# Optimization experiments

Measured on AMD Instinct MI355X. Metric: run time of the kernel, lower is better.

The kernel has to match this reference:

```python
import jax, jax.numpy as jnp
import numpy as np
import itertools

B, G, FEAT, IMG = 2048, 8, 512, 1024
SCALES = list(range(G, 1, -1))  # [8,7,6,5,4,3,2]
SUBSAMPLE = 12


def setup_inputs() -> dict:
    key = jax.random.key(0)
    keys = jax.random.split(key, 1 + 2 * len(SCALES))
    rng = np.random.default_rng(0)
    inp = {"input": jax.random.normal(keys[0], (B, G, FEAT), dtype=jnp.float32)}
    for i, scale in enumerate(SCALES):
        perms = np.array(list(itertools.permutations(range(G), scale)), dtype=np.int32)
        n_sub = min(SUBSAMPLE, len(perms))
        sel = rng.choice(len(perms), n_sub, replace=False)
        inp[f"perms{i}"] = jnp.asarray(perms[sel])  # [n_sub, scale] int32
        lim = 1.0 / np.sqrt(scale * FEAT)
        inp[f"W{i}"] = jax.random.uniform(keys[1 + 2 * i], (IMG, scale * FEAT), minval=-lim, maxval=lim, dtype=jnp.float32)
        inp[f"b{i}"] = jax.random.uniform(keys[2 + 2 * i], (IMG,), minval=-lim, maxval=lim, dtype=jnp.float32)
    return inp


def _forward(input, perms_list, W_list, b_list):
    outs = []
    for perms, W, b in zip(perms_list, W_list, b_list):
        # gather: [B, n_sub, scale, FEAT] -> [B, n_sub, scale*FEAT]
        g = input[:, perms, :]
        g = g.reshape(g.shape[0], g.shape[1], -1)
        # batched linear over all subsamples, then mean over subsamples
        y = jnp.einsum('bsf,df->bsd', g, W) + b  # [B, n_sub, IMG]
        outs.append(y.mean(axis=1))
    return jnp.concatenate(outs, axis=1)  # [B, len(SCALES)*IMG]


def reference(input, perms0, W0, b0, perms1, W1, b1, perms2, W2, b2,
              perms3, W3, b3, perms4, W4, b4, perms5, W5, b5, perms6, W6, b6):
    perms_list = [perms0, perms1, perms2, perms3, perms4, perms5, perms6]
    W_list = [W0, W1, W2, W3, W4, W5, W6]
    b_list = [b0, b1, b2, b3, b4, b5, b6]
    return _forward(input, perms_list, W_list, b_list)
```

## Files before the change

kernel.cpp:

```cpp
#include <hip/hip_runtime.h>

typedef unsigned short u16;
typedef __bf16 bf16x8 __attribute__((ext_vector_type(8)));
typedef float f32x4 __attribute__((ext_vector_type(4)));

__device__ __forceinline__ u16 f2bf(float f) {
  unsigned int u = __float_as_uint(f);
  return (u16)((u + 0x7fffu + ((u >> 16) & 1u)) >> 16);
}


__global__ __launch_bounds__(256) void k_prep(
    const float* __restrict__ x,
    const int* p0, const int* p1, const int* p2, const int* p3,
    const int* p4, const int* p5, const int* p6,
    const float* W0, const float* W1, const float* W2, const float* W3,
    const float* W4, const float* W5, const float* W6,
    u16* __restrict__ Xb16, u16* __restrict__ Wtil) {
  __shared__ float sC[64];
  const int bid = blockIdx.x;
  const int t = threadIdx.x;
  if (bid < 1792) {
    const int r0 = bid << 2;
    const int i = r0 >> 10;
    const int scale = 8 - i;
    const int K = scale << 9;
    const int d0 = r0 - (i << 10);
    if (t < 64) {
      const int g = t >> 3, j = t & 7;
      float v = 0.f;
      if (j < scale) {
        const int* p = (i == 0) ? p0 : (i == 1) ? p1 : (i == 2) ? p2 :
                       (i == 3) ? p3 : (i == 4) ? p4 : (i == 5) ? p5 : p6;
        int cnt = 0;
        for (int s = 0; s < 12; ++s) cnt += (p[s * scale + j] == g) ? 1 : 0;
        v = (float)cnt * (1.0f / 12.0f);
      }
      sC[t] = v;
    }
    __syncthreads();
    const float* Wi = (i == 0) ? W0 : (i == 1) ? W1 : (i == 2) ? W2 :
                      (i == 3) ? W3 : (i == 4) ? W4 : (i == 5) ? W5 : W6;
    const int u = t & 63;
    const int gq = t >> 6;
    u16* dst = Wtil + ((size_t)r0 << 12);
    for (int r = 0; r < 4; ++r) {
      const float* wrow = Wi + (size_t)(d0 + r) * K;
      float a0[8], a1[8];
#pragma unroll
      for (int e = 0; e < 8; ++e) { a0[e] = 0.f; a1[e] = 0.f; }
      for (int j = 0; j < scale; ++j) {
        const float* wp = wrow + j * 512 + (u << 3);
        const float4 wa = *reinterpret_cast<const float4*>(wp);
        const float4 wb = *reinterpret_cast<const float4*>(wp + 4);
        const float c0 = sC[(gq << 4) + j];
        const float c1 = sC[(gq << 4) + 8 + j];
        a0[0] += c0 * wa.x; a0[1] += c0 * wa.y; a0[2] += c0 * wa.z; a0[3] += c0 * wa.w;
        a0[4] += c0 * wb.x; a0[5] += c0 * wb.y; a0[6] += c0 * wb.z; a0[7] += c0 * wb.w;
        a1[0] += c1 * wa.x; a1[1] += c1 * wa.y; a1[2] += c1 * wa.z; a1[3] += c1 * wa.w;
        a1[4] += c1 * wb.x; a1[5] += c1 * wb.y; a1[6] += c1 * wb.z; a1[7] += c1 * wb.w;
      }
      uint4 o0, o1;
      o0.x = (unsigned)f2bf(a0[0]) | ((unsigned)f2bf(a0[1]) << 16);
      o0.y = (unsigned)f2bf(a0[2]) | ((unsigned)f2bf(a0[3]) << 16);
      o0.z = (unsigned)f2bf(a0[4]) | ((unsigned)f2bf(a0[5]) << 16);
      o0.w = (unsigned)f2bf(a0[6]) | ((unsigned)f2bf(a0[7]) << 16);
      o1.x = (unsigned)f2bf(a1[0]) | ((unsigned)f2bf(a1[1]) << 16);
      o1.y = (unsigned)f2bf(a1[2]) | ((unsigned)f2bf(a1[3]) << 16);
      o1.z = (unsigned)f2bf(a1[4]) | ((unsigned)f2bf(a1[5]) << 16);
      o1.w = (unsigned)f2bf(a1[6]) | ((unsigned)f2bf(a1[7]) << 16);
      u16* drow = dst + ((size_t)r << 12) + (gq << 10) + (u << 3);
      *reinterpret_cast<uint4*>(drow) = o0;
      *reinterpret_cast<uint4*>(drow + 512) = o1;
    }
  } else {
    const int tid0 = ((bid - 1792) << 8) | t;
    const float4* X4 = reinterpret_cast<const float4*>(x);
    uint4* O = reinterpret_cast<uint4*>(Xb16);
#pragma unroll 4
    for (int it = 0; it < 16; ++it) {
      const int e = tid0 + (it << 16);
      const float4 a = X4[(size_t)e * 2];
      const float4 c = X4[(size_t)e * 2 + 1];
      uint4 o;
      o.x = (unsigned)f2bf(a.x) | ((unsigned)f2bf(a.y) << 16);
      o.y = (unsigned)f2bf(a.z) | ((unsigned)f2bf(a.w) << 16);
      o.z = (unsigned)f2bf(c.x) | ((unsigned)f2bf(c.y) << 16);
      o.w = (unsigned)f2bf(c.z) | ((unsigned)f2bf(c.w) << 16);
      O[e] = o;
    }
  }
}

__device__ __forceinline__ void gl_lds16(const u16* g, u16* l) {
  __builtin_amdgcn_global_load_lds(
      (const __attribute__((address_space(1))) void*)g,
      (__attribute__((address_space(3))) void*)l, 16, 0, 0);
}

#define WAIT_VM2   0x0F72
#define WAIT_VM0   0x0F70
#define WAIT_LGKM0 0xC07F

#define MFMA_Q(MB, NB, AV, BV)                                               \
  _Pragma("unroll")                                                          \
  for (int q_ = 0; q_ < 4; ++q_) {                                           \
    _Pragma("unroll")                                                        \
    for (int n_ = 0; n_ < 2; ++n_) {                                         \
      acc[(MB) + q_][(NB) + n_] = __builtin_amdgcn_mfma_f32_16x16x32_bf16(   \
          AV[q_][0], BV[n_][0], acc[(MB) + q_][(NB) + n_], 0, 0, 0);         \
      acc[(MB) + q_][(NB) + n_] = __builtin_amdgcn_mfma_f32_16x16x32_bf16(   \
          AV[q_][1], BV[n_][1], acc[(MB) + q_][(NB) + n_], 0, 0, 0);         \
    }                                                                        \
  }

#define RD_A4(DB, QB)                                                        \
  _Pragma("unroll")                                                          \
  for (int q_ = 0; q_ < 4; ++q_) {                                           \
    aR[q_][0] = *reinterpret_cast<const bf16x8*>(lds + (DB) + offA[(QB) + q_]);         \
    aR[q_][1] = *reinterpret_cast<const bf16x8*>(lds + (DB) + (offA[(QB) + q_] ^ 32));  \
  }

#define RD_B2(DB, ARR, FB)                                                   \
  _Pragma("unroll")                                                          \
  for (int n_ = 0; n_ < 2; ++n_) {                                           \
    ARR[n_][0] = *reinterpret_cast<const bf16x8*>(lds + (DB) + offB[(FB) + n_]);        \
    ARR[n_][1] = *reinterpret_cast<const bf16x8*>(lds + (DB) + (offB[(FB) + n_] ^ 32)); \
  }

__global__ __launch_bounds__(512, 2) void k_gemm(
    const u16* __restrict__ A, const u16* __restrict__ Bm,
    const float* b0, const float* b1, const float* b2, const float* b3,
    const float* b4, const float* b5, const float* b6,
    float* __restrict__ out) {
  __shared__ u16 lds[65536];
  const int bid = blockIdx.x;
  const int blockM = (bid & 7) * 256;
  const int blockN = (bid >> 3) * 256;

  const int tid = threadIdx.x;
  const int lane = tid & 63;
  const int wid = tid >> 6;
  const int wr = wid >> 2;
  const int wc = wid & 3;
  const int quad = lane >> 4;
  const int l15 = lane & 15;

  const int srow = tid >> 3;
  const int sslot = tid & 7;
  const int gch = (sslot - srow) & 7;
  const u16* gA0 = A + (size_t)(blockM + srow) * 4096 + gch * 8;
  const u16* gB0 = Bm + (size_t)(blockN + srow) * 4096 + gch * 8;

  int offA[8], offB[4];
#pragma unroll
  for (int q = 0; q < 8; ++q) {
    const int r = q * 16 + l15;
    offA[q] = wr * 8192 + r * 64 + ((quad + r) & 7) * 8;
  }
#pragma unroll
  for (int f = 0; f < 4; ++f) {
    const int r = (wc & 1) * 64 + f * 16 + l15;
    offB[f] = 16384 + (wc >> 1) * 8192 + r * 64 + ((quad + r) & 7) * 8;
  }

  f32x4 acc[8][4];
#pragma unroll
  for (int m = 0; m < 8; ++m)
#pragma unroll
    for (int n = 0; n < 4; ++n) {
      f32x4 z = {0.f, 0.f, 0.f, 0.f};
      acc[m][n] = z;
    }

  auto stage = [&](int mat, int h, int t, int db) {
    const u16* g = (mat ? gB0 : gA0) + (size_t)h * (128 * 4096) + (size_t)t * 64;
    u16* l = lds + db + mat * 16384 + h * 8192 + (tid << 3);
    gl_lds16(g, l);
    gl_lds16(g + (size_t)(64 * 4096), l + 4096);
  };

  stage(0, 0, 0, 0); stage(0, 1, 0, 0); stage(1, 0, 0, 0); stage(1, 1, 0, 0);
  stage(0, 0, 1, 32768);
  __builtin_amdgcn_s_waitcnt(WAIT_VM2);
  __builtin_amdgcn_s_barrier();

  bf16x8 aR[4][2], bL[2][2], bH[2][2];

  for (int j = 0; j < 32; ++j) {
    const int t1 = 2 * j + 1;
    const int t2 = (j < 31) ? 2 * j + 2 : 63;
    const int t3 = (j < 31) ? 2 * j + 3 : 63;

    RD_A4(0, 0) RD_B2(0, bL, 0)
    stage(0, 1, t1, 32768);
    __builtin_amdgcn_s_barrier();
    __builtin_amdgcn_s_waitcnt(WAIT_LGKM0);
    __builtin_amdgcn_s_setprio(1);
    MFMA_Q(0, 0, aR, bL)
    __builtin_amdgcn_s_setprio(0);
    __builtin_amdgcn_s_barrier();

    RD_B2(0, bH, 2)
    stage(1, 0, t1, 32768);
    __builtin_amdgcn_s_barrier();
    __builtin_amdgcn_s_waitcnt(WAIT_LGKM0);
    __builtin_amdgcn_s_setprio(1);
    MFMA_Q(0, 2, aR, bH)
    __builtin_amdgcn_s_setprio(0);
    __builtin_amdgcn_s_barrier();

    RD_A4(0, 4)
    stage(1, 1, t1, 32768);
    __builtin_amdgcn_s_barrier();
    __builtin_amdgcn_s_waitcnt(WAIT_LGKM0);
    __builtin_amdgcn_s_setprio(1);
    MFMA_Q(4, 2, aR, bH)
    __builtin_amdgcn_s_setprio(0);
    __builtin_amdgcn_s_barrier();

    stage(0, 0, t2, 0);
    __builtin_amdgcn_s_barrier();
    __builtin_amdgcn_s_setprio(1);
    MFMA_Q(4, 0, aR, bL)
    __builtin_amdgcn_s_setprio(0);
    __builtin_amdgcn_s_waitcnt(WAIT_VM2);
    __builtin_amdgcn_s_barrier();

    RD_A4(32768, 0) RD_B2(32768, bL, 0)
    stage(0, 1, t2, 0);
    __builtin_amdgcn_s_barrier();
    __builtin_amdgcn_s_waitcnt(WAIT_LGKM0);
    __builtin_amdgcn_s_setprio(1);
    MFMA_Q(0, 0, aR, bL)
    __builtin_amdgcn_s_setprio(0);
    __builtin_amdgcn_s_barrier();

    RD_B2(32768, bH, 2)
    stage(1, 0, t2, 0);
    __builtin_amdgcn_s_barrier();
    __builtin_amdgcn_s_waitcnt(WAIT_LGKM0);
    __builtin_amdgcn_s_setprio(1);
    MFMA_Q(0, 2, aR, bH)
    __builtin_amdgcn_s_setprio(0);
    __builtin_amdgcn_s_barrier();

    RD_A4(32768, 4)
    stage(1, 1, t2, 0);
    __builtin_amdgcn_s_barrier();
    __builtin_amdgcn_s_waitcnt(WAIT_LGKM0);
    __builtin_amdgcn_s_setprio(1);
    MFMA_Q(4, 2, aR, bH)
    __builtin_amdgcn_s_setprio(0);
    __builtin_amdgcn_s_barrier();

    stage(0, 0, t3, 32768);
    __builtin_amdgcn_s_barrier();
    __builtin_amdgcn_s_setprio(1);
    MFMA_Q(4, 0, aR, bL)
    __builtin_amdgcn_s_setprio(0);
    __builtin_amdgcn_s_waitcnt(WAIT_VM2);
    __builtin_amdgcn_s_barrier();
  }
  __builtin_amdgcn_s_waitcnt(WAIT_VM0);

  const int isc = blockN >> 10;
  const float* bi = (isc == 0) ? b0 : (isc == 1) ? b1 : (isc == 2) ? b2 :
                    (isc == 3) ? b3 : (isc == 4) ? b4 : (isc == 5) ? b5 : b6;
#pragma unroll
  for (int nf = 0; nf < 4; ++nf) {
    const int ncol = blockN + wc * 64 + nf * 16 + l15;
    const float bias = bi[ncol & 1023];
#pragma unroll
    for (int mq = 0; mq < 8; ++mq) {
      const int mbase = blockM + wr * 128 + mq * 16 + quad * 4;
#pragma unroll
      for (int reg = 0; reg < 4; ++reg)
        out[(size_t)(mbase + reg) * 7168 + ncol] = acc[mq][nf][reg] + bias;
    }
  }
}

extern "C" void kernel_launch(void* const* d_in, const int* in_sizes, int n_in,
                              void* d_out, int out_size, void* d_ws, size_t ws_size,
                              hipStream_t stream) {
  const float* input = (const float*)d_in[0];
  const int* perms[7];
  const float* W[7];
  const float* bias[7];
  for (int i = 0; i < 7; ++i) {
    perms[i] = (const int*)d_in[1 + 3 * i];
    W[i]     = (const float*)d_in[2 + 3 * i];
    bias[i]  = (const float*)d_in[3 + 3 * i];
  }
  char* ws = (char*)d_ws;
  u16* Xb16 = (u16*)ws;
  u16* Wtil = (u16*)(ws + (size_t)2048 * 4096 * 2);

  k_prep<<<2048, 256, 0, stream>>>(input,
                                   perms[0], perms[1], perms[2], perms[3],
                                   perms[4], perms[5], perms[6],
                                   W[0], W[1], W[2], W[3], W[4], W[5], W[6],
                                   Xb16, Wtil);
  k_gemm<<<224, 512, 0, stream>>>(Xb16, Wtil,
                                  bias[0], bias[1], bias[2], bias[3],
                                  bias[4], bias[5], bias[6],
                                  (float*)d_out);
}
```

Baseline: 303.4 us.

## Reassign warp tiles to quadrant layout and deepen global-to-LDS prefetch pipeline

Warps now own a 64x32 sub-tile in each of four 128x128 quadrants of the block tile, replacing the previous 128x64 strip. Each MFMA phase consumes one quadrant's A/B halves, so the stage order and buffers are rearranged to follow that. The prologue issues more stages ahead and the loop waits with a looser vmcnt, keeping more global loads in flight, and the last iteration is peeled with a tapering wait sequence. This aims to hide global-load latency better, at the cost of more outstanding loads and more intricate wait/barrier accounting that must stay correct.

```diff
diff --git a/kernel.cpp b/kernel.cpp
--- a/kernel.cpp
+++ b/kernel.cpp
@@ -98,35 +98,43 @@
       (__attribute__((address_space(3))) void*)l, 16, 0, 0);
 }
 
+#define WAIT_VM10  0x0F7A
+#define WAIT_VM8   0x0F78
+#define WAIT_VM4   0x0F74
 #define WAIT_VM2   0x0F72
 #define WAIT_VM0   0x0F70
 #define WAIT_LGKM0 0xC07F
 
-#define MFMA_Q(MB, NB, AV, BV)                                               \
+#define MFMA_Q(QD, AV, BV)                                                   \
   _Pragma("unroll")                                                          \
-  for (int q_ = 0; q_ < 4; ++q_) {                                           \
+  for (int mf_ = 0; mf_ < 4; ++mf_) {                                        \
     _Pragma("unroll")                                                        \
-    for (int n_ = 0; n_ < 2; ++n_) {                                         \
-      acc[(MB) + q_][(NB) + n_] = __builtin_amdgcn_mfma_f32_16x16x32_bf16(   \
-          AV[q_][0], BV[n_][0], acc[(MB) + q_][(NB) + n_], 0, 0, 0);         \
-      acc[(MB) + q_][(NB) + n_] = __builtin_amdgcn_mfma_f32_16x16x32_bf16(   \
-          AV[q_][1], BV[n_][1], acc[(MB) + q_][(NB) + n_], 0, 0, 0);         \
+    for (int nf_ = 0; nf_ < 2; ++nf_) {                                      \
+      acc[QD][mf_][nf_] = __builtin_amdgcn_mfma_f32_16x16x32_bf16(           \
+          AV[mf_][0], BV[nf_][0], acc[QD][mf_][nf_], 0, 0, 0);               \
+      acc[QD][mf_][nf_] = __builtin_amdgcn_mfma_f32_16x16x32_bf16(           \
+          AV[mf_][1], BV[nf_][1], acc[QD][mf_][nf_], 0, 0, 0);               \
     }                                                                        \
   }
 
-#define RD_A4(DB, QB)                                                        \
+#define RD_A(BASE)                                                           \
   _Pragma("unroll")                                                          \
-  for (int q_ = 0; q_ < 4; ++q_) {                                           \
-    aR[q_][0] = *reinterpret_cast<const bf16x8*>(lds + (DB) + offA[(QB) + q_]);         \
-    aR[q_][1] = *reinterpret_cast<const bf16x8*>(lds + (DB) + (offA[(QB) + q_] ^ 32));  \
-  }
-
-#define RD_B2(DB, ARR, FB)                                                   \
+  for (int mf_ = 0; mf_ < 4; ++mf_) {                                        \
+    aR[mf_][0] = *reinterpret_cast<const bf16x8*>(lds + (BASE) + offA[mf_]);        \
+    aR[mf_][1] = *reinterpret_cast<const bf16x8*>(lds + (BASE) + (offA[mf_] ^ 32)); \
+  }
+
+#define RD_B(BASE, ARR)                                                      \
   _Pragma("unroll")                                                          \
-  for (int n_ = 0; n_ < 2; ++n_) {                                           \
-    ARR[n_][0] = *reinterpret_cast<const bf16x8*>(lds + (DB) + offB[(FB) + n_]);        \
-    ARR[n_][1] = *reinterpret_cast<const bf16x8*>(lds + (DB) + (offB[(FB) + n_] ^ 32)); \
-  }
+  for (int nf_ = 0; nf_ < 2; ++nf_) {                                        \
+    ARR[nf_][0] = *reinterpret_cast<const bf16x8*>(lds + (BASE) + offB[nf_]);        \
+    ARR[nf_][1] = *reinterpret_cast<const bf16x8*>(lds + (BASE) + (offB[nf_] ^ 32)); \
+  }
+
+#define PH_BAR  __builtin_amdgcn_s_barrier()
+#define PH_LGKM __builtin_amdgcn_s_waitcnt(WAIT_LGKM0)
+#define PRIO1   __builtin_amdgcn_s_setprio(1)
+#define PRIO0   __builtin_amdgcn_s_setprio(0)
 
 __global__ __launch_bounds__(512, 2) void k_gemm(
     const u16* __restrict__ A, const u16* __restrict__ Bm,
@@ -141,8 +149,8 @@
   const int tid = threadIdx.x;
   const int lane = tid & 63;
   const int wid = tid >> 6;
-  const int wr = wid >> 2;
-  const int wc = wid & 3;
+  const int wm = (wid >> 2) * 64;
+  const int wn = (wid & 3) * 32;
   const int quad = lane >> 4;
   const int l15 = lane & 15;
 
@@ -152,26 +160,28 @@
   const u16* gA0 = A + (size_t)(blockM + srow) * 4096 + gch * 8;
   const u16* gB0 = Bm + (size_t)(blockN + srow) * 4096 + gch * 8;
 
-  int offA[8], offB[4];
-#pragma unroll
-  for (int q = 0; q < 8; ++q) {
-    const int r = q * 16 + l15;
-    offA[q] = wr * 8192 + r * 64 + ((quad + r) & 7) * 8;
-  }
-#pragma unroll
-  for (int f = 0; f < 4; ++f) {
-    const int r = (wc & 1) * 64 + f * 16 + l15;
-    offB[f] = 16384 + (wc >> 1) * 8192 + r * 64 + ((quad + r) & 7) * 8;
-  }
-
-  f32x4 acc[8][4];
-#pragma unroll
-  for (int m = 0; m < 8; ++m)
-#pragma unroll
-    for (int n = 0; n < 4; ++n) {
-      f32x4 z = {0.f, 0.f, 0.f, 0.f};
-      acc[m][n] = z;
-    }
+  int offA[4], offB[2];
+#pragma unroll
+  for (int mf = 0; mf < 4; ++mf) {
+    const int r = wm + mf * 16 + l15;
+    offA[mf] = r * 64 + ((quad + r) & 7) * 8;
+  }
+#pragma unroll
+  for (int nf = 0; nf < 2; ++nf) {
+    const int r = wn + nf * 16 + l15;
+    offB[nf] = 16384 + r * 64 + ((quad + r) & 7) * 8;
+  }
+
+  f32x4 acc[4][4][2];
+#pragma unroll
+  for (int q = 0; q < 4; ++q)
+#pragma unroll
+    for (int m = 0; m < 4; ++m)
+#pragma unroll
+      for (int n = 0; n < 2; ++n) {
+        f32x4 z = {0.f, 0.f, 0.f, 0.f};
+        acc[q][m][n] = z;
+      }
 
   auto stage = [&](int mat, int h, int t, int db) {
     const u16* g = (mat ? gB0 : gA0) + (size_t)h * (128 * 4096) + (size_t)t * 64;
@@ -180,103 +190,107 @@
     gl_lds16(g + (size_t)(64 * 4096), l + 4096);
   };
 
-  stage(0, 0, 0, 0); stage(0, 1, 0, 0); stage(1, 0, 0, 0); stage(1, 1, 0, 0);
-  stage(0, 0, 1, 32768);
-  __builtin_amdgcn_s_waitcnt(WAIT_VM2);
-  __builtin_amdgcn_s_barrier();
+  stage(0, 0, 0, 0); stage(1, 0, 0, 0); stage(1, 1, 0, 0); stage(0, 1, 0, 0);
+  stage(0, 0, 1, 32768); stage(1, 0, 1, 32768); stage(1, 1, 1, 32768);
+  __builtin_amdgcn_s_waitcnt(WAIT_VM10);
+  PH_BAR;
 
   bf16x8 aR[4][2], bL[2][2], bH[2][2];
 
-  for (int j = 0; j < 32; ++j) {
+  for (int j = 0; j < 31; ++j) {
     const int t1 = 2 * j + 1;
-    const int t2 = (j < 31) ? 2 * j + 2 : 63;
-    const int t3 = (j < 31) ? 2 * j + 3 : 63;
-
-    RD_A4(0, 0) RD_B2(0, bL, 0)
+    const int t2 = 2 * j + 2;
+    const int t3 = 2 * j + 3;
+
+    RD_A(0) RD_B(0, bL)
     stage(0, 1, t1, 32768);
-    __builtin_amdgcn_s_barrier();
-    __builtin_amdgcn_s_waitcnt(WAIT_LGKM0);
-    __builtin_amdgcn_s_setprio(1);
-    MFMA_Q(0, 0, aR, bL)
-    __builtin_amdgcn_s_setprio(0);
-    __builtin_amdgcn_s_barrier();
-
-    RD_B2(0, bH, 2)
-    stage(1, 0, t1, 32768);
-    __builtin_amdgcn_s_barrier();
-    __builtin_amdgcn_s_waitcnt(WAIT_LGKM0);
-    __builtin_amdgcn_s_setprio(1);
-    MFMA_Q(0, 2, aR, bH)
-    __builtin_amdgcn_s_setprio(0);
-    __builtin_amdgcn_s_barrier();
-
-    RD_A4(0, 4)
-    stage(1, 1, t1, 32768);
-    __builtin_amdgcn_s_barrier();
-    __builtin_amdgcn_s_waitcnt(WAIT_LGKM0);
-    __builtin_amdgcn_s_setprio(1);
-    MFMA_Q(4, 2, aR, bH)
-    __builtin_amdgcn_s_setprio(0);
-    __builtin_amdgcn_s_barrier();
-
+    PH_BAR; PH_LGKM; PRIO1; MFMA_Q(0, aR, bL) PRIO0;
+    __builtin_amdgcn_s_waitcnt(WAIT_VM10); PH_BAR;
+
+    RD_B(8192, bH)
     stage(0, 0, t2, 0);
-    __builtin_amdgcn_s_barrier();
-    __builtin_amdgcn_s_setprio(1);
-    MFMA_Q(4, 0, aR, bL)
-    __builtin_amdgcn_s_setprio(0);
-    __builtin_amdgcn_s_waitcnt(WAIT_VM2);
-    __builtin_amdgcn_s_barrier();
-
-    RD_A4(32768, 0) RD_B2(32768, bL, 0)
+    PH_BAR; PH_LGKM; PRIO1; MFMA_Q(1, aR, bH) PRIO0;
+    __builtin_amdgcn_s_waitcnt(WAIT_VM10); PH_BAR;
+
+    RD_A(8192)
+    stage(1, 0, t2, 0);
+    PH_BAR; PH_LGKM; PRIO1; MFMA_Q(2, aR, bH) PRIO0;
+    PH_BAR;
+
+    stage(1, 1, t2, 0);
+    PH_BAR; PRIO1; MFMA_Q(3, aR, bL) PRIO0;
+    __builtin_amdgcn_s_waitcnt(WAIT_VM10); PH_BAR;
+
+    RD_A(32768) RD_B(32768, bL)
     stage(0, 1, t2, 0);
-    __builtin_amdgcn_s_barrier();
-    __builtin_amdgcn_s_waitcnt(WAIT_LGKM0);
-    __builtin_amdgcn_s_setprio(1);
-    MFMA_Q(0, 0, aR, bL)
-    __builtin_amdgcn_s_setprio(0);
-    __builtin_amdgcn_s_barrier();
-
-    RD_B2(32768, bH, 2)
-    stage(1, 0, t2, 0);
-    __builtin_amdgcn_s_barrier();
-    __builtin_amdgcn_s_waitcnt(WAIT_LGKM0);
-    __builtin_amdgcn_s_setprio(1);
-    MFMA_Q(0, 2, aR, bH)
-    __builtin_amdgcn_s_setprio(0);
-    __builtin_amdgcn_s_barrier();
-
-    RD_A4(32768, 4)
-    stage(1, 1, t2, 0);
-    __builtin_amdgcn_s_barrier();
-    __builtin_amdgcn_s_waitcnt(WAIT_LGKM0);
-    __builtin_amdgcn_s_setprio(1);
-    MFMA_Q(4, 2, aR, bH)
-    __builtin_amdgcn_s_setprio(0);
-    __builtin_amdgcn_s_barrier();
-
+    PH_BAR; PH_LGKM; PRIO1; MFMA_Q(0, aR, bL) PRIO0;
+    __builtin_amdgcn_s_waitcnt(WAIT_VM10); PH_BAR;
+
+    RD_B(32768 + 8192, bH)
     stage(0, 0, t3, 32768);
-    __builtin_amdgcn_s_barrier();
-    __builtin_amdgcn_s_setprio(1);
-    MFMA_Q(4, 0, aR, bL)
-    __builtin_amdgcn_s_setprio(0);
-    __builtin_amdgcn_s_waitcnt(WAIT_VM2);
-    __builtin_amdgcn_s_barrier();
-  }
-  __builtin_amdgcn_s_waitcnt(WAIT_VM0);
+    PH_BAR; PH_LGKM; PRIO1; MFMA_Q(1, aR, bH) PRIO0;
+    __builtin_amdgcn_s_waitcnt(WAIT_VM10); PH_BAR;
+
+    RD_A(32768 + 8192)
+    stage(1, 0, t3, 32768);
+    PH_BAR; PH_LGKM; PRIO1; MFMA_Q(2, aR, bH) PRIO0;
+    PH_BAR;
+
+    stage(1, 1, t3, 32768);
+    PH_BAR; PRIO1; MFMA_Q(3, aR, bL) PRIO0;
+    __builtin_amdgcn_s_waitcnt(WAIT_VM10); PH_BAR;
+  }
+
+  {
+    RD_A(0) RD_B(0, bL)
+    stage(0, 1, 63, 32768);
+    PH_BAR; PH_LGKM; PRIO1; MFMA_Q(0, aR, bL) PRIO0;
+    __builtin_amdgcn_s_waitcnt(WAIT_VM10); PH_BAR;
+
+    RD_B(8192, bH)
+    PH_BAR; PH_LGKM; PRIO1; MFMA_Q(1, aR, bH) PRIO0;
+    __builtin_amdgcn_s_waitcnt(WAIT_VM8); PH_BAR;
+
+    RD_A(8192)
+    PH_BAR; PH_LGKM; PRIO1; MFMA_Q(2, aR, bH) PRIO0;
+    PH_BAR;
+
+    PH_BAR; PRIO1; MFMA_Q(3, aR, bL) PRIO0;
+    __builtin_amdgcn_s_waitcnt(WAIT_VM4); PH_BAR;
+
+    RD_A(32768) RD_B(32768, bL)
+    PH_BAR; PH_LGKM; PRIO1; MFMA_Q(0, aR, bL) PRIO0;
+    __builtin_amdgcn_s_waitcnt(WAIT_VM2); PH_BAR;
+
+    RD_B(32768 + 8192, bH)
+    PH_BAR; PH_LGKM; PRIO1; MFMA_Q(1, aR, bH) PRIO0;
+    __builtin_amdgcn_s_waitcnt(WAIT_VM0); PH_BAR;
+
+    RD_A(32768 + 8192)
+    PH_BAR; PH_LGKM; PRIO1; MFMA_Q(2, aR, bH) PRIO0;
+    PH_BAR;
+
+    PRIO1; MFMA_Q(3, aR, bL) PRIO0;
+  }
 
   const int isc = blockN >> 10;
   const float* bi = (isc == 0) ? b0 : (isc == 1) ? b1 : (isc == 2) ? b2 :
                     (isc == 3) ? b3 : (isc == 4) ? b4 : (isc == 5) ? b5 : b6;
 #pragma unroll
-  for (int nf = 0; nf < 4; ++nf) {
-    const int ncol = blockN + wc * 64 + nf * 16 + l15;
-    const float bias = bi[ncol & 1023];
-#pragma unroll
-    for (int mq = 0; mq < 8; ++mq) {
-      const int mbase = blockM + wr * 128 + mq * 16 + quad * 4;
-#pragma unroll
-      for (int reg = 0; reg < 4; ++reg)
-        out[(size_t)(mbase + reg) * 7168 + ncol] = acc[mq][nf][reg] + bias;
+  for (int qd = 0; qd < 4; ++qd) {
+    const int Mq = (qd >= 2) ? 128 : 0;
+    const int Nq = (qd == 1 || qd == 2) ? 128 : 0;
+#pragma unroll
+    for (int nf = 0; nf < 2; ++nf) {
+      const int ncol = blockN + Nq + wn + nf * 16 + l15;
+      const float bias = bi[ncol & 1023];
+#pragma unroll
+      for (int mf = 0; mf < 4; ++mf) {
+        const int mbase = blockM + Mq + wm + mf * 16 + quad * 4;
+#pragma unroll
+        for (int reg = 0; reg < 4; ++reg)
+          out[(size_t)(mbase + reg) * 7168 + ncol] = acc[qd][mf][nf][reg] + bias;
+      }
     }
   }
 }
```

After: 298.2 us. No clear change (-1.7%).

## Prefetch A fragments across phases and peel final GEMM iteration

Applied to the files above, without the earlier changes.

Restructures the GEMM main loop to software-pipeline LDS reads of A fragments. The next half-tile's A registers are loaded before the preceding MFMA group, using separate register sets (aPI/aPO/aH). The last iteration is peeled so it no longer issues redundant loads of tile 63. VM4 waits replace some VM2 waits, and the stage order in the prologue changes. The aim is to hide LDS read latency behind MFMAs, at the cost of more registers and possible spills under launch_bounds(512,2).

```diff
diff --git a/kernel.cpp b/kernel.cpp
--- a/kernel.cpp
+++ b/kernel.cpp
@@ -98,9 +98,27 @@
       (__attribute__((address_space(3))) void*)l, 16, 0, 0);
 }
 
-#define WAIT_VM2   0x0F72
-#define WAIT_VM0   0x0F70
-#define WAIT_LGKM0 0xC07F
+#define VM4 __builtin_amdgcn_s_waitcnt(0x0F74)
+#define VM2 __builtin_amdgcn_s_waitcnt(0x0F72)
+#define VM0 __builtin_amdgcn_s_waitcnt(0x0F70)
+#define LG0 __builtin_amdgcn_s_waitcnt(0xC07F)
+#define BAR __builtin_amdgcn_s_barrier()
+#define P1  __builtin_amdgcn_s_setprio(1)
+#define P0  __builtin_amdgcn_s_setprio(0)
+
+#define RD_A4(dst, DB, QB)                                                   \
+  _Pragma("unroll")                                                          \
+  for (int q_ = 0; q_ < 4; ++q_) {                                           \
+    dst[q_][0] = *reinterpret_cast<const bf16x8*>(lds + (DB) + offA[(QB) + q_]);         \
+    dst[q_][1] = *reinterpret_cast<const bf16x8*>(lds + (DB) + (offA[(QB) + q_] ^ 32)); \
+  }
+
+#define RD_B2(ARR, DB, FB)                                                   \
+  _Pragma("unroll")                                                          \
+  for (int n_ = 0; n_ < 2; ++n_) {                                           \
+    ARR[n_][0] = *reinterpret_cast<const bf16x8*>(lds + (DB) + offB[(FB) + n_]);         \
+    ARR[n_][1] = *reinterpret_cast<const bf16x8*>(lds + (DB) + (offB[(FB) + n_] ^ 32)); \
+  }
 
 #define MFMA_Q(MB, NB, AV, BV)                                               \
   _Pragma("unroll")                                                          \
@@ -114,20 +132,6 @@
     }                                                                        \
   }
 
-#define RD_A4(DB, QB)                                                        \
-  _Pragma("unroll")                                                          \
-  for (int q_ = 0; q_ < 4; ++q_) {                                           \
-    aR[q_][0] = *reinterpret_cast<const bf16x8*>(lds + (DB) + offA[(QB) + q_]);         \
-    aR[q_][1] = *reinterpret_cast<const bf16x8*>(lds + (DB) + (offA[(QB) + q_] ^ 32));  \
-  }
-
-#define RD_B2(DB, ARR, FB)                                                   \
-  _Pragma("unroll")                                                          \
-  for (int n_ = 0; n_ < 2; ++n_) {                                           \
-    ARR[n_][0] = *reinterpret_cast<const bf16x8*>(lds + (DB) + offB[(FB) + n_]);        \
-    ARR[n_][1] = *reinterpret_cast<const bf16x8*>(lds + (DB) + (offB[(FB) + n_] ^ 32)); \
-  }
-
 __global__ __launch_bounds__(512, 2) void k_gemm(
     const u16* __restrict__ A, const u16* __restrict__ Bm,
     const float* b0, const float* b1, const float* b2, const float* b3,
@@ -166,11 +170,11 @@
 
   f32x4 acc[8][4];
 #pragma unroll
-  for (int m = 0; m < 8; ++m)
-#pragma unroll
-    for (int n = 0; n < 4; ++n) {
+  for (int q = 0; q < 8; ++q)
+#pragma unroll
+    for (int c = 0; c < 4; ++c) {
       f32x4 z = {0.f, 0.f, 0.f, 0.f};
-      acc[m][n] = z;
+      acc[q][c] = z;
     }
 
   auto stage = [&](int mat, int h, int t, int db) {
@@ -180,103 +184,101 @@
     gl_lds16(g + (size_t)(64 * 4096), l + 4096);
   };
 
-  stage(0, 0, 0, 0); stage(0, 1, 0, 0); stage(1, 0, 0, 0); stage(1, 1, 0, 0);
+  bf16x8 aPI[4][2], aPO[4][2], aH[4][2], bL[2][2], bH[2][2];
+
+  stage(0, 0, 0, 0); stage(1, 0, 0, 0); stage(1, 1, 0, 0); stage(0, 1, 0, 0);
   stage(0, 0, 1, 32768);
-  __builtin_amdgcn_s_waitcnt(WAIT_VM2);
-  __builtin_amdgcn_s_barrier();
-
-  bf16x8 aR[4][2], bL[2][2], bH[2][2];
-
-  for (int j = 0; j < 32; ++j) {
+  VM2;
+  BAR;
+  RD_A4(aPI, 0, 0)
+
+  for (int j = 0; j < 31; ++j) {
     const int t1 = 2 * j + 1;
-    const int t2 = (j < 31) ? 2 * j + 2 : 63;
-    const int t3 = (j < 31) ? 2 * j + 3 : 63;
-
-    RD_A4(0, 0) RD_B2(0, bL, 0)
+    const int t2 = 2 * j + 2;
+    const int t3 = 2 * j + 3;
+
+    RD_B2(bL, 0, 0)
     stage(0, 1, t1, 32768);
-    __builtin_amdgcn_s_barrier();
-    __builtin_amdgcn_s_waitcnt(WAIT_LGKM0);
-    __builtin_amdgcn_s_setprio(1);
-    MFMA_Q(0, 0, aR, bL)
-    __builtin_amdgcn_s_setprio(0);
-    __builtin_amdgcn_s_barrier();
-
-    RD_B2(0, bH, 2)
+    BAR; LG0; P1; MFMA_Q(0, 0, aPI, bL) P0;
+    BAR;
+
+    RD_B2(bH, 0, 2)
     stage(1, 0, t1, 32768);
-    __builtin_amdgcn_s_barrier();
-    __builtin_amdgcn_s_waitcnt(WAIT_LGKM0);
-    __builtin_amdgcn_s_setprio(1);
-    MFMA_Q(0, 2, aR, bH)
-    __builtin_amdgcn_s_setprio(0);
-    __builtin_amdgcn_s_barrier();
-
-    RD_A4(0, 4)
+    BAR; LG0; P1; MFMA_Q(0, 2, aPI, bH) P0;
+    BAR;
+
+    RD_A4(aH, 0, 4)
     stage(1, 1, t1, 32768);
-    __builtin_amdgcn_s_barrier();
-    __builtin_amdgcn_s_waitcnt(WAIT_LGKM0);
-    __builtin_amdgcn_s_setprio(1);
-    MFMA_Q(4, 2, aR, bH)
-    __builtin_amdgcn_s_setprio(0);
-    __builtin_amdgcn_s_barrier();
-
+    BAR; LG0; P1; MFMA_Q(4, 2, aH, bH) P0;
+    VM4; BAR;
+
+    RD_A4(aPO, 32768, 0)
     stage(0, 0, t2, 0);
-    __builtin_amdgcn_s_barrier();
-    __builtin_amdgcn_s_setprio(1);
-    MFMA_Q(4, 0, aR, bL)
-    __builtin_amdgcn_s_setprio(0);
-    __builtin_amdgcn_s_waitcnt(WAIT_VM2);
-    __builtin_amdgcn_s_barrier();
-
-    RD_A4(32768, 0) RD_B2(32768, bL, 0)
+    BAR; P1; MFMA_Q(4, 0, aH, bL) P0;
+    VM2; BAR;
+
+    RD_B2(bL, 32768, 0)
     stage(0, 1, t2, 0);
-    __builtin_amdgcn_s_barrier();
-    __builtin_amdgcn_s_waitcnt(WAIT_LGKM0);
-    __builtin_amdgcn_s_setprio(1);
-    MFMA_Q(0, 0, aR, bL)
-    __builtin_amdgcn_s_setprio(0);
-    __builtin_amdgcn_s_barrier();
-
-    RD_B2(32768, bH, 2)
+    BAR; LG0; P1; MFMA_Q(0, 0, aPO, bL) P0;
+    BAR;
+
+    RD_B2(bH, 32768, 2)
     stage(1, 0, t2, 0);
-    __builtin_amdgcn_s_barrier();
-    __builtin_amdgcn_s_waitcnt(WAIT_LGKM0);
-    __builtin_amdgcn_s_setprio(1);
-    MFMA_Q(0, 2, aR, bH)
-    __builtin_amdgcn_s_setprio(0);
-    __builtin_amdgcn_s_barrier();
-
-    RD_A4(32768, 4)
+    BAR; LG0; P1; MFMA_Q(0, 2, aPO, bH) P0;
+    BAR;
+
+    RD_A4(aH, 32768, 4)
     stage(1, 1, t2, 0);
-    __builtin_amdgcn_s_barrier();
-    __builtin_amdgcn_s_waitcnt(WAIT_LGKM0);
-    __builtin_amdgcn_s_setprio(1);
-    MFMA_Q(4, 2, aR, bH)
-    __builtin_amdgcn_s_setprio(0);
-    __builtin_amdgcn_s_barrier();
-
+    BAR; LG0; P1; MFMA_Q(4, 2, aH, bH) P0;
+    VM4; BAR;
+
+    RD_A4(aPI, 0, 0)
     stage(0, 0, t3, 32768);
-    __builtin_amdgcn_s_barrier();
-    __builtin_amdgcn_s_setprio(1);
-    MFMA_Q(4, 0, aR, bL)
-    __builtin_amdgcn_s_setprio(0);
-    __builtin_amdgcn_s_waitcnt(WAIT_VM2);
-    __builtin_amdgcn_s_barrier();
-  }
-  __builtin_amdgcn_s_waitcnt(WAIT_VM0);
+    BAR; P1; MFMA_Q(4, 0, aH, bL) P0;
+    VM2; BAR;
+  }
+
+  {
+    RD_B2(bL, 0, 0)
+    stage(0, 1, 63, 32768);
+    BAR; LG0; P1; MFMA_Q(0, 0, aPI, bL) P0;
+    BAR;
+    RD_B2(bH, 0, 2)
+    stage(1, 0, 63, 32768);
+    BAR; LG0; P1; MFMA_Q(0, 2, aPI, bH) P0;
+    BAR;
+    RD_A4(aH, 0, 4)
+    stage(1, 1, 63, 32768);
+    BAR; LG0; P1; MFMA_Q(4, 2, aH, bH) P0;
+    VM4; BAR;
+    RD_A4(aPO, 32768, 0)
+    BAR; P1; MFMA_Q(4, 0, aH, bL) P0;
+    VM0; BAR;
+    RD_B2(bL, 32768, 0)
+    BAR; LG0; P1; MFMA_Q(0, 0, aPO, bL) P0;
+    BAR;
+    RD_B2(bH, 32768, 2)
+    BAR; LG0; P1; MFMA_Q(0, 2, aPO, bH) P0;
+    BAR;
+    RD_A4(aH, 32768, 4)
+    BAR; LG0; P1; MFMA_Q(4, 2, aH, bH) P0;
+    BAR;
+    P1; MFMA_Q(4, 0, aH, bL) P0;
+  }
 
   const int isc = blockN >> 10;
   const float* bi = (isc == 0) ? b0 : (isc == 1) ? b1 : (isc == 2) ? b2 :
                     (isc == 3) ? b3 : (isc == 4) ? b4 : (isc == 5) ? b5 : b6;
 #pragma unroll
-  for (int nf = 0; nf < 4; ++nf) {
-    const int ncol = blockN + wc * 64 + nf * 16 + l15;
+  for (int f = 0; f < 4; ++f) {
+    const int ncol = blockN + (wc >> 1) * 128 + (wc & 1) * 64 + f * 16 + l15;
     const float bias = bi[ncol & 1023];
 #pragma unroll
-    for (int mq = 0; mq < 8; ++mq) {
-      const int mbase = blockM + wr * 128 + mq * 16 + quad * 4;
+    for (int q = 0; q < 8; ++q) {
+      const int mbase = blockM + wr * 128 + q * 16 + quad * 4;
 #pragma unroll
       for (int reg = 0; reg < 4; ++reg)
-        out[(size_t)(mbase + reg) * 7168 + ncol] = acc[mq][nf][reg] + bias;
+        out[(size_t)(mbase + reg) * 7168 + ncol] = acc[q][f][reg] + bias;
     }
   }
 }
```

After: 304.9 us. No clear change (+0.5%).
